# Kernel optimization log

Measured on AMD Instinct MI355X. Metric: run time of the kernel, lower is better.

## Reference

```python
import jax, jax.numpy as jnp
import numpy as np

N, E, F, H = 50000, 400000, 128, 512


def setup_inputs() -> dict:
    key = jax.random.key(0)
    k1, k2, k3 = jax.random.split(key, 3)
    x = jax.random.normal(k1, (N, F), dtype=jnp.float32)
    edge_index = jax.random.randint(k2, (2, E), 0, N, dtype=jnp.int64)
    W = jax.random.normal(k3, (H, F), dtype=jnp.float32) * 0.05  # GCNConv linear weight [out, in]
    b = jnp.zeros((H,), dtype=jnp.float32)
    alpha = jnp.full((H,), 0.25, dtype=jnp.float32)  # PReLU default init per channel
    return {"x": x, "edge_index": edge_index, "W": W, "b": b, "alpha": alpha}


def reference(x, edge_index, W, b, alpha):
    n = x.shape[0]
    # GCNConv: linear transform first (no bias inside the matmul)
    h = x @ W.T  # [N, H]
    # add self-loops (GCNConv default add_self_loops=True)
    loops = jnp.arange(n, dtype=edge_index.dtype)
    row = jnp.concatenate([edge_index[0], loops])  # source
    col = jnp.concatenate([edge_index[1], loops])  # target
    # symmetric degree normalization: deg from edge weights (all ones) summed at targets
    deg = jax.ops.segment_sum(jnp.ones_like(col, dtype=h.dtype), col, num_segments=n)
    dinv = jnp.where(deg > 0, jax.lax.rsqrt(jnp.maximum(deg, 1.0)) * (deg > 0), 0.0)
    dinv = jnp.where(deg > 0, 1.0 / jnp.sqrt(jnp.maximum(deg, 1e-12)), 0.0)
    norm = dinv[row] * dinv[col]  # [E+N]
    # gather source features, scale, scatter-add to targets
    msgs = h[row] * norm[:, None]  # [E+N, H] -- the memory-bound gather
    out = jax.ops.segment_sum(msgs, col, num_segments=n) + b  # [N, H]
    # PReLU with per-channel alpha
    return jnp.where(out > 0, out, alpha * out)
```

## Files before the change

### kernel.cpp

```cpp
#include <hip/hip_runtime.h>


#define F_IN 128
#define H_OUT 512

typedef __bf16 bf16x8 __attribute__((ext_vector_type(8)));
typedef float  f32x4  __attribute__((ext_vector_type(4)));

__global__ __launch_bounds__(256) void cast_bf16_kernel(const float* __restrict__ src,
                                                        __bf16* __restrict__ dst, int n8) {
    int i = blockIdx.x * 256 + threadIdx.x;
    if (i >= n8) return;
    float4 a = ((const float4*)src)[i * 2];
    float4 b = ((const float4*)src)[i * 2 + 1];
    bf16x8 v;
    v[0] = (__bf16)a.x; v[1] = (__bf16)a.y; v[2] = (__bf16)a.z; v[3] = (__bf16)a.w;
    v[4] = (__bf16)b.x; v[5] = (__bf16)b.y; v[6] = (__bf16)b.z; v[7] = (__bf16)b.w;
    ((bf16x8*)dst)[i] = v;
}

__global__ __launch_bounds__(256) void scale_cast_kernel(const float* __restrict__ x,
                                                         const float* __restrict__ dinv,
                                                         __bf16* __restrict__ xs, int n8) {
    int i = blockIdx.x * 256 + threadIdx.x;
    if (i >= n8) return;
    float dv = dinv[i >> 4];
    float4 a = ((const float4*)x)[i * 2];
    float4 b = ((const float4*)x)[i * 2 + 1];
    bf16x8 v;
    v[0] = (__bf16)(a.x * dv); v[1] = (__bf16)(a.y * dv);
    v[2] = (__bf16)(a.z * dv); v[3] = (__bf16)(a.w * dv);
    v[4] = (__bf16)(b.x * dv); v[5] = (__bf16)(b.y * dv);
    v[6] = (__bf16)(b.z * dv); v[7] = (__bf16)(b.w * dv);
    ((bf16x8*)xs)[i] = v;
}

__global__ __launch_bounds__(256) void count_deg_kernel(const int* __restrict__ col,
                                                        unsigned* __restrict__ deg, int E) {
    int e = blockIdx.x * 256 + threadIdx.x;
    if (e < E) atomicAdd(&deg[col[e]], 1u);
}

__global__ __launch_bounds__(256) void deg_reduce_kernel(const unsigned* __restrict__ deg,
                                                         unsigned* __restrict__ partial, int n) {
    __shared__ unsigned wsum[4];
    const int t = threadIdx.x;
    const int i0 = blockIdx.x * 1024 + t * 4;
    unsigned s = 0;
    if (i0 + 3 < n) {
        uint4 v = *(const uint4*)(deg + i0);
        s = v.x + v.y + v.z + v.w;
    } else {
        #pragma unroll
        for (int j = 0; j < 4; ++j) if (i0 + j < n) s += deg[i0 + j];
    }
    #pragma unroll
    for (int o = 32; o > 0; o >>= 1) s += __shfl_down(s, (unsigned)o, 64);
    if ((t & 63) == 0) wsum[t >> 6] = s;
    __syncthreads();
    if (t == 0) partial[blockIdx.x] = wsum[0] + wsum[1] + wsum[2] + wsum[3];
}

__global__ __launch_bounds__(64) void scan_partials_kernel(const unsigned* __restrict__ partial,
                                                           unsigned* __restrict__ offs, int nb) {
    const int t = threadIdx.x;
    unsigned v = (t < nb) ? partial[t] : 0u;
    unsigned x = v;
    #pragma unroll
    for (int o = 1; o < 64; o <<= 1) {
        unsigned y = __shfl_up(x, (unsigned)o, 64);
        if (t >= o) x += y;
    }
    if (t < nb) offs[t] = x - v;
}

__global__ __launch_bounds__(256) void scan_apply_kernel(const unsigned* __restrict__ deg,
                                                         const unsigned* __restrict__ offs,
                                                         int* __restrict__ rowptr,
                                                         float* __restrict__ dinv,
                                                         unsigned* __restrict__ cursor,
                                                         int n, int E) {
    __shared__ unsigned wsum[4];
    const int t = threadIdx.x, lane = t & 63, wid = t >> 6;
    const int i0 = blockIdx.x * 1024 + t * 4;
    unsigned d[4] = {0u, 0u, 0u, 0u};
    if (i0 + 3 < n) {
        uint4 v = *(const uint4*)(deg + i0);
        d[0] = v.x; d[1] = v.y; d[2] = v.z; d[3] = v.w;
    } else {
        #pragma unroll
        for (int j = 0; j < 4; ++j) if (i0 + j < n) d[j] = deg[i0 + j];
    }
    unsigned s = d[0] + d[1] + d[2] + d[3];
    unsigned x = s;
    #pragma unroll
    for (int o = 1; o < 64; o <<= 1) {
        unsigned y = __shfl_up(x, (unsigned)o, 64);
        if (lane >= o) x += y;
    }
    if (lane == 63) wsum[wid] = x;
    __syncthreads();
    unsigned wprev = 0;
    for (int q = 0; q < wid; ++q) wprev += wsum[q];
    unsigned base = offs[blockIdx.x] + wprev + (x - s);
    unsigned run = 0;
    #pragma unroll
    for (int j = 0; j < 4; ++j) {
        int i = i0 + j;
        if (i < n) {
            rowptr[i] = (int)(base + run);
            dinv[i]   = rsqrtf((float)(d[j] + 1u));
            cursor[i] = 0u;
        }
        run += d[j];
    }
    if (blockIdx.x == 0 && t == 0) rowptr[n] = E;
}

__global__ __launch_bounds__(256) void fill_csr_kernel(const int* __restrict__ row,
                                                       const int* __restrict__ col,
                                                       const int* __restrict__ rowptr,
                                                       unsigned* __restrict__ cursor,
                                                       int* __restrict__ adj, int E) {
    int e = blockIdx.x * 256 + threadIdx.x;
    if (e >= E) return;
    int c = col[e];
    unsigned p = atomicAdd(&cursor[c], 1u);
    adj[rowptr[c] + (int)p] = row[e];
}

__global__ __launch_bounds__(256) void gather_agg_kernel(const int* __restrict__ rowptr,
                                                         const int* __restrict__ adj,
                                                         const __bf16* __restrict__ xs,
                                                         const float* __restrict__ dinv,
                                                         __bf16* __restrict__ ag, int N) {
    const int t = threadIdx.x;
    const int node = blockIdx.x * 16 + (t >> 4);
    if (node >= N) return;
    const int li = t & 15;

    const bf16x8* xs8 = (const bf16x8*)xs;
    bf16x8 sv = xs8[(size_t)node * 16 + li];
    float acc[8];
    #pragma unroll
    for (int q = 0; q < 8; ++q) acc[q] = (float)sv[q];

    const int s = rowptr[node];
    const int e = rowptr[node + 1];
    int j = s;
    for (; j + 3 < e; j += 4) {
        int r0 = adj[j], r1 = adj[j + 1], r2 = adj[j + 2], r3 = adj[j + 3];
        bf16x8 v0 = xs8[(size_t)r0 * 16 + li];
        bf16x8 v1 = xs8[(size_t)r1 * 16 + li];
        bf16x8 v2 = xs8[(size_t)r2 * 16 + li];
        bf16x8 v3 = xs8[(size_t)r3 * 16 + li];
        #pragma unroll
        for (int q = 0; q < 8; ++q)
            acc[q] += ((float)v0[q] + (float)v1[q]) + ((float)v2[q] + (float)v3[q]);
    }
    for (; j < e; ++j) {
        int r0 = adj[j];
        bf16x8 v0 = xs8[(size_t)r0 * 16 + li];
        #pragma unroll
        for (int q = 0; q < 8; ++q) acc[q] += (float)v0[q];
    }

    const float dv = dinv[node];
    bf16x8 o;
    #pragma unroll
    for (int q = 0; q < 8; ++q) o[q] = (__bf16)(acc[q] * dv);
    ((bf16x8*)ag)[(size_t)node * 16 + li] = o;
}

__global__ __launch_bounds__(256) void gemm_mfma_kernel(const __bf16* __restrict__ ag,
                                                        const __bf16* __restrict__ Wb,
                                                        const float* __restrict__ bias,
                                                        const float* __restrict__ alpha,
                                                        float* __restrict__ out, int N) {
    __shared__ __bf16 As[128][136];
    __shared__ __bf16 Bs[128][136];

    const int rb = blockIdx.x * 128;
    const int cb = blockIdx.y * 128;
    const int t  = threadIdx.x;

    #pragma unroll
    for (int i = 0; i < 8; ++i) {
        int c  = i * 256 + t;
        int r  = c >> 4;
        int k8 = (c & 15) * 8;
        bf16x8 v;
        #pragma unroll
        for (int j = 0; j < 8; ++j) v[j] = (__bf16)0.0f;
        if (rb + r < N) v = *(const bf16x8*)(ag + (size_t)(rb + r) * F_IN + k8);
        *(bf16x8*)&As[r][k8] = v;
    }
    #pragma unroll
    for (int i = 0; i < 8; ++i) {
        int c  = i * 256 + t;
        int r  = c >> 4;
        int k8 = (c & 15) * 8;
        bf16x8 v = *(const bf16x8*)(Wb + (size_t)(cb + r) * F_IN + k8);
        *(bf16x8*)&Bs[r][k8] = v;
    }
    __syncthreads();

    const int w    = t >> 6;
    const int lane = t & 63;
    const int lrow = lane & 15;
    const int lk   = (lane >> 4) * 8;

    f32x4 acc[2][8] = {};
    #pragma unroll
    for (int ks = 0; ks < 4; ++ks) {
        const int k0 = ks * 32 + lk;
        bf16x8 a0 = *(const bf16x8*)&As[w * 32 + lrow][k0];
        bf16x8 a1 = *(const bf16x8*)&As[w * 32 + 16 + lrow][k0];
        #pragma unroll
        for (int tn = 0; tn < 8; ++tn) {
            bf16x8 bfr = *(const bf16x8*)&Bs[tn * 16 + lrow][k0];
            acc[0][tn] = __builtin_amdgcn_mfma_f32_16x16x32_bf16(a0, bfr, acc[0][tn], 0, 0, 0);
            acc[1][tn] = __builtin_amdgcn_mfma_f32_16x16x32_bf16(a1, bfr, acc[1][tn], 0, 0, 0);
        }
    }

    float bb[8], aa[8];
    #pragma unroll
    for (int tn = 0; tn < 8; ++tn) {
        int n = cb + tn * 16 + lrow;
        bb[tn] = bias[n];
        aa[tn] = alpha[n];
    }
    const int rloc = (lane >> 4) * 4;
    #pragma unroll
    for (int tm = 0; tm < 2; ++tm) {
        #pragma unroll
        for (int r = 0; r < 4; ++r) {
            int m = rb + w * 32 + tm * 16 + rloc + r;
            if (m >= N) continue;
            #pragma unroll
            for (int tn = 0; tn < 8; ++tn) {
                int n = cb + tn * 16 + lrow;
                float v = acc[tm][tn][r] + bb[tn];
                v = v > 0.f ? v : aa[tn] * v;
                out[(size_t)m * H_OUT + n] = v;
            }
        }
    }
}

extern "C" void kernel_launch(void* const* d_in, const int* in_sizes, int n_in,
                              void* d_out, int out_size, void* d_ws, size_t ws_size,
                              hipStream_t stream) {
    const float* x     = (const float*)d_in[0];
    const int*   ei    = (const int*)d_in[1];
    const float* W     = (const float*)d_in[2];
    const float* b     = (const float*)d_in[3];
    const float* alpha = (const float*)d_in[4];
    float*       out   = (float*)d_out;

    const int N = in_sizes[0] / F_IN;
    const int E = in_sizes[1] / 2;
    const int* row = ei;
    const int* col = ei + E;
    const int NB = (N + 1023) / 1024;

    char* wsb = (char*)d_ws;
    size_t off = 0;
    __bf16* xs = (__bf16*)(wsb + off);  off += (size_t)N * F_IN * 2;     off = (off + 63) & ~(size_t)63;
    __bf16* ag = (__bf16*)(wsb + off);  off += (size_t)N * F_IN * 2;     off = (off + 63) & ~(size_t)63;
    __bf16* Wb = (__bf16*)(wsb + off);  off += (size_t)H_OUT * F_IN * 2; off = (off + 63) & ~(size_t)63;
    unsigned* deg    = (unsigned*)(wsb + off);  off += (size_t)N * 4;
    unsigned* cursor = (unsigned*)(wsb + off);  off += (size_t)N * 4;
    float*    dinv   = (float*)(wsb + off);     off += (size_t)N * 4;
    int*      rowptr = (int*)(wsb + off);       off += (size_t)(N + 1) * 4;
    off = (off + 63) & ~(size_t)63;
    unsigned* partial = (unsigned*)(wsb + off); off += (size_t)NB * 4;
    unsigned* offs    = (unsigned*)(wsb + off); off += (size_t)NB * 4;
    off = (off + 63) & ~(size_t)63;
    int* adj = (int*)(wsb + off);

    hipMemsetAsync(deg, 0, (size_t)N * 4, stream);

    int nw8 = H_OUT * F_IN / 8;
    cast_bf16_kernel<<<(nw8 + 255) / 256, 256, 0, stream>>>(W, Wb, nw8);

    count_deg_kernel<<<(E + 255) / 256, 256, 0, stream>>>(col, deg, E);
    deg_reduce_kernel<<<NB, 256, 0, stream>>>(deg, partial, N);
    scan_partials_kernel<<<1, 64, 0, stream>>>(partial, offs, NB);
    scan_apply_kernel<<<NB, 256, 0, stream>>>(deg, offs, rowptr, dinv, cursor, N, E);
    fill_csr_kernel<<<(E + 255) / 256, 256, 0, stream>>>(row, col, rowptr, cursor, adj, E);

    int nx8 = N * F_IN / 8;
    scale_cast_kernel<<<(nx8 + 255) / 256, 256, 0, stream>>>(x, dinv, xs, nx8);

    gather_agg_kernel<<<(N + 15) / 16, 256, 0, stream>>>(rowptr, adj, xs, dinv, ag, N);

    dim3 ggrid((N + 127) / 128, H_OUT / 128);
    gemm_mfma_kernel<<<ggrid, 256, 0, stream>>>(ag, Wb, b, alpha, out, N);
}
```

Baseline: 220.1 us.

## Merge prep kernels, replace scan with atomic segment allocation, move dinv into gather

Fuses the W cast, the x cast and the degree counting into one launch. The three-kernel prefix scan is replaced by a per-wavefront scan that reserves its segment base with an atomic on a global counter, so CSR segments are no longer in node order. fill_csr writes straight to the cursor, and the final cursor value marks each segment's end. Because dinv is now computed after x is cast, the source-side scaling moves into the gather as a per-neighbor dinv load, which adds extra scattered loads in exchange for fewer launches.

```diff
diff --git a/kernel.cpp b/kernel.cpp
--- a/kernel.cpp
+++ b/kernel.cpp
@@ -7,129 +7,76 @@
 typedef __bf16 bf16x8 __attribute__((ext_vector_type(8)));
 typedef float  f32x4  __attribute__((ext_vector_type(4)));
 
-__global__ __launch_bounds__(256) void cast_bf16_kernel(const float* __restrict__ src,
-                                                        __bf16* __restrict__ dst, int n8) {
-    int i = blockIdx.x * 256 + threadIdx.x;
-    if (i >= n8) return;
-    float4 a = ((const float4*)src)[i * 2];
-    float4 b = ((const float4*)src)[i * 2 + 1];
-    bf16x8 v;
-    v[0] = (__bf16)a.x; v[1] = (__bf16)a.y; v[2] = (__bf16)a.z; v[3] = (__bf16)a.w;
-    v[4] = (__bf16)b.x; v[5] = (__bf16)b.y; v[6] = (__bf16)b.z; v[7] = (__bf16)b.w;
-    ((bf16x8*)dst)[i] = v;
-}
-
-__global__ __launch_bounds__(256) void scale_cast_kernel(const float* __restrict__ x,
-                                                         const float* __restrict__ dinv,
-                                                         __bf16* __restrict__ xs, int n8) {
-    int i = blockIdx.x * 256 + threadIdx.x;
-    if (i >= n8) return;
-    float dv = dinv[i >> 4];
-    float4 a = ((const float4*)x)[i * 2];
-    float4 b = ((const float4*)x)[i * 2 + 1];
-    bf16x8 v;
-    v[0] = (__bf16)(a.x * dv); v[1] = (__bf16)(a.y * dv);
-    v[2] = (__bf16)(a.z * dv); v[3] = (__bf16)(a.w * dv);
-    v[4] = (__bf16)(b.x * dv); v[5] = (__bf16)(b.y * dv);
-    v[6] = (__bf16)(b.z * dv); v[7] = (__bf16)(b.w * dv);
-    ((bf16x8*)xs)[i] = v;
-}
-
-__global__ __launch_bounds__(256) void count_deg_kernel(const int* __restrict__ col,
-                                                        unsigned* __restrict__ deg, int E) {
-    int e = blockIdx.x * 256 + threadIdx.x;
-    if (e < E) atomicAdd(&deg[col[e]], 1u);
-}
-
-__global__ __launch_bounds__(256) void deg_reduce_kernel(const unsigned* __restrict__ deg,
-                                                         unsigned* __restrict__ partial, int n) {
-    __shared__ unsigned wsum[4];
-    const int t = threadIdx.x;
-    const int i0 = blockIdx.x * 1024 + t * 4;
-    unsigned s = 0;
-    if (i0 + 3 < n) {
-        uint4 v = *(const uint4*)(deg + i0);
-        s = v.x + v.y + v.z + v.w;
+__global__ __launch_bounds__(256) void prep_kernel(const float* __restrict__ W,
+                                                   __bf16* __restrict__ Wb, int nw8,
+                                                   const float* __restrict__ x,
+                                                   __bf16* __restrict__ xs, int nx8,
+                                                   const int* __restrict__ col,
+                                                   unsigned* __restrict__ deg, int E,
+                                                   int NWB, int NXB) {
+    const int b = blockIdx.x, t = threadIdx.x;
+    if (b < NWB) {
+        int i = b * 256 + t;
+        if (i >= nw8) return;
+        float4 a0 = ((const float4*)W)[i * 2];
+        float4 a1 = ((const float4*)W)[i * 2 + 1];
+        bf16x8 v;
+        v[0] = (__bf16)a0.x; v[1] = (__bf16)a0.y; v[2] = (__bf16)a0.z; v[3] = (__bf16)a0.w;
+        v[4] = (__bf16)a1.x; v[5] = (__bf16)a1.y; v[6] = (__bf16)a1.z; v[7] = (__bf16)a1.w;
+        ((bf16x8*)Wb)[i] = v;
+    } else if (b < NWB + NXB) {
+        int i = (b - NWB) * 256 + t;
+        if (i >= nx8) return;
+        float4 a0 = ((const float4*)x)[i * 2];
+        float4 a1 = ((const float4*)x)[i * 2 + 1];
+        bf16x8 v;
+        v[0] = (__bf16)a0.x; v[1] = (__bf16)a0.y; v[2] = (__bf16)a0.z; v[3] = (__bf16)a0.w;
+        v[4] = (__bf16)a1.x; v[5] = (__bf16)a1.y; v[6] = (__bf16)a1.z; v[7] = (__bf16)a1.w;
+        ((bf16x8*)xs)[i] = v;
     } else {
-        #pragma unroll
-        for (int j = 0; j < 4; ++j) if (i0 + j < n) s += deg[i0 + j];
-    }
-    #pragma unroll
-    for (int o = 32; o > 0; o >>= 1) s += __shfl_down(s, (unsigned)o, 64);
-    if ((t & 63) == 0) wsum[t >> 6] = s;
-    __syncthreads();
-    if (t == 0) partial[blockIdx.x] = wsum[0] + wsum[1] + wsum[2] + wsum[3];
-}
-
-__global__ __launch_bounds__(64) void scan_partials_kernel(const unsigned* __restrict__ partial,
-                                                           unsigned* __restrict__ offs, int nb) {
-    const int t = threadIdx.x;
-    unsigned v = (t < nb) ? partial[t] : 0u;
-    unsigned x = v;
-    #pragma unroll
-    for (int o = 1; o < 64; o <<= 1) {
-        unsigned y = __shfl_up(x, (unsigned)o, 64);
-        if (t >= o) x += y;
-    }
-    if (t < nb) offs[t] = x - v;
-}
-
-__global__ __launch_bounds__(256) void scan_apply_kernel(const unsigned* __restrict__ deg,
-                                                         const unsigned* __restrict__ offs,
-                                                         int* __restrict__ rowptr,
-                                                         float* __restrict__ dinv,
-                                                         unsigned* __restrict__ cursor,
-                                                         int n, int E) {
-    __shared__ unsigned wsum[4];
-    const int t = threadIdx.x, lane = t & 63, wid = t >> 6;
-    const int i0 = blockIdx.x * 1024 + t * 4;
-    unsigned d[4] = {0u, 0u, 0u, 0u};
-    if (i0 + 3 < n) {
-        uint4 v = *(const uint4*)(deg + i0);
-        d[0] = v.x; d[1] = v.y; d[2] = v.z; d[3] = v.w;
-    } else {
-        #pragma unroll
-        for (int j = 0; j < 4; ++j) if (i0 + j < n) d[j] = deg[i0 + j];
-    }
-    unsigned s = d[0] + d[1] + d[2] + d[3];
-    unsigned x = s;
+        int e = (b - NWB - NXB) * 256 + t;
+        if (e < E) atomicAdd(&deg[col[e]], 1u);
+    }
+}
+
+__global__ __launch_bounds__(256) void assign_kernel(const unsigned* __restrict__ deg,
+                                                     unsigned* __restrict__ total,
+                                                     int* __restrict__ rowptr,
+                                                     unsigned* __restrict__ cursor,
+                                                     float* __restrict__ dinv, int n) {
+    const int i = blockIdx.x * 256 + threadIdx.x;
+    const int lane = threadIdx.x & 63;
+    unsigned d = (i < n) ? deg[i] : 0u;
+    unsigned x = d;
     #pragma unroll
     for (int o = 1; o < 64; o <<= 1) {
         unsigned y = __shfl_up(x, (unsigned)o, 64);
         if (lane >= o) x += y;
     }
-    if (lane == 63) wsum[wid] = x;
-    __syncthreads();
-    unsigned wprev = 0;
-    for (int q = 0; q < wid; ++q) wprev += wsum[q];
-    unsigned base = offs[blockIdx.x] + wprev + (x - s);
-    unsigned run = 0;
-    #pragma unroll
-    for (int j = 0; j < 4; ++j) {
-        int i = i0 + j;
-        if (i < n) {
-            rowptr[i] = (int)(base + run);
-            dinv[i]   = rsqrtf((float)(d[j] + 1u));
-            cursor[i] = 0u;
-        }
-        run += d[j];
-    }
-    if (blockIdx.x == 0 && t == 0) rowptr[n] = E;
+    unsigned tot = __shfl(x, 63, 64);
+    unsigned wb = 0;
+    if (lane == 63) wb = atomicAdd(total, tot);
+    wb = __shfl(wb, 63, 64);
+    if (i < n) {
+        unsigned start = wb + x - d;
+        rowptr[i] = (int)start;
+        cursor[i] = start;
+        dinv[i]   = rsqrtf((float)(d + 1u));
+    }
 }
 
 __global__ __launch_bounds__(256) void fill_csr_kernel(const int* __restrict__ row,
                                                        const int* __restrict__ col,
-                                                       const int* __restrict__ rowptr,
                                                        unsigned* __restrict__ cursor,
                                                        int* __restrict__ adj, int E) {
     int e = blockIdx.x * 256 + threadIdx.x;
     if (e >= E) return;
-    int c = col[e];
-    unsigned p = atomicAdd(&cursor[c], 1u);
-    adj[rowptr[c] + (int)p] = row[e];
+    unsigned p = atomicAdd(&cursor[col[e]], 1u);
+    adj[p] = row[e];
 }
 
 __global__ __launch_bounds__(256) void gather_agg_kernel(const int* __restrict__ rowptr,
+                                                         const unsigned* __restrict__ cursor,
                                                          const int* __restrict__ adj,
                                                          const __bf16* __restrict__ xs,
                                                          const float* __restrict__ dinv,
@@ -140,35 +87,38 @@
     const int li = t & 15;
 
     const bf16x8* xs8 = (const bf16x8*)xs;
+    const float dvn = dinv[node];
     bf16x8 sv = xs8[(size_t)node * 16 + li];
     float acc[8];
     #pragma unroll
-    for (int q = 0; q < 8; ++q) acc[q] = (float)sv[q];
+    for (int q = 0; q < 8; ++q) acc[q] = dvn * (float)sv[q];
 
     const int s = rowptr[node];
-    const int e = rowptr[node + 1];
+    const int e = (int)cursor[node];
     int j = s;
     for (; j + 3 < e; j += 4) {
         int r0 = adj[j], r1 = adj[j + 1], r2 = adj[j + 2], r3 = adj[j + 3];
+        float w0 = dinv[r0], w1 = dinv[r1], w2 = dinv[r2], w3 = dinv[r3];
         bf16x8 v0 = xs8[(size_t)r0 * 16 + li];
         bf16x8 v1 = xs8[(size_t)r1 * 16 + li];
         bf16x8 v2 = xs8[(size_t)r2 * 16 + li];
         bf16x8 v3 = xs8[(size_t)r3 * 16 + li];
         #pragma unroll
         for (int q = 0; q < 8; ++q)
-            acc[q] += ((float)v0[q] + (float)v1[q]) + ((float)v2[q] + (float)v3[q]);
+            acc[q] += (w0 * (float)v0[q] + w1 * (float)v1[q]) +
+                      (w2 * (float)v2[q] + w3 * (float)v3[q]);
     }
     for (; j < e; ++j) {
         int r0 = adj[j];
+        float w0 = dinv[r0];
         bf16x8 v0 = xs8[(size_t)r0 * 16 + li];
         #pragma unroll
-        for (int q = 0; q < 8; ++q) acc[q] += (float)v0[q];
-    }
-
-    const float dv = dinv[node];
+        for (int q = 0; q < 8; ++q) acc[q] += w0 * (float)v0[q];
+    }
+
     bf16x8 o;
     #pragma unroll
-    for (int q = 0; q < 8; ++q) o[q] = (__bf16)(acc[q] * dv);
+    for (int q = 0; q < 8; ++q) o[q] = (__bf16)(acc[q] * dvn);
     ((bf16x8*)ag)[(size_t)node * 16 + li] = o;
 }
 
@@ -263,39 +213,32 @@
     const int E = in_sizes[1] / 2;
     const int* row = ei;
     const int* col = ei + E;
-    const int NB = (N + 1023) / 1024;
 
     char* wsb = (char*)d_ws;
     size_t off = 0;
     __bf16* xs = (__bf16*)(wsb + off);  off += (size_t)N * F_IN * 2;     off = (off + 63) & ~(size_t)63;
     __bf16* ag = (__bf16*)(wsb + off);  off += (size_t)N * F_IN * 2;     off = (off + 63) & ~(size_t)63;
     __bf16* Wb = (__bf16*)(wsb + off);  off += (size_t)H_OUT * F_IN * 2; off = (off + 63) & ~(size_t)63;
-    unsigned* deg    = (unsigned*)(wsb + off);  off += (size_t)N * 4;
+    unsigned* deg    = (unsigned*)(wsb + off);  off += (size_t)(N + 1) * 4;
     unsigned* cursor = (unsigned*)(wsb + off);  off += (size_t)N * 4;
     float*    dinv   = (float*)(wsb + off);     off += (size_t)N * 4;
-    int*      rowptr = (int*)(wsb + off);       off += (size_t)(N + 1) * 4;
-    off = (off + 63) & ~(size_t)63;
-    unsigned* partial = (unsigned*)(wsb + off); off += (size_t)NB * 4;
-    unsigned* offs    = (unsigned*)(wsb + off); off += (size_t)NB * 4;
+    int*      rowptr = (int*)(wsb + off);       off += (size_t)N * 4;
     off = (off + 63) & ~(size_t)63;
     int* adj = (int*)(wsb + off);
-
-    hipMemsetAsync(deg, 0, (size_t)N * 4, stream);
-
-    int nw8 = H_OUT * F_IN / 8;
-    cast_bf16_kernel<<<(nw8 + 255) / 256, 256, 0, stream>>>(W, Wb, nw8);
-
-    count_deg_kernel<<<(E + 255) / 256, 256, 0, stream>>>(col, deg, E);
-    deg_reduce_kernel<<<NB, 256, 0, stream>>>(deg, partial, N);
-    scan_partials_kernel<<<1, 64, 0, stream>>>(partial, offs, NB);
-    scan_apply_kernel<<<NB, 256, 0, stream>>>(deg, offs, rowptr, dinv, cursor, N, E);
-    fill_csr_kernel<<<(E + 255) / 256, 256, 0, stream>>>(row, col, rowptr, cursor, adj, E);
-
-    int nx8 = N * F_IN / 8;
-    scale_cast_kernel<<<(nx8 + 255) / 256, 256, 0, stream>>>(x, dinv, xs, nx8);
-
-    gather_agg_kernel<<<(N + 15) / 16, 256, 0, stream>>>(rowptr, adj, xs, dinv, ag, N);
-
+    unsigned* total = deg + N;
+
+    const int nw8 = H_OUT * F_IN / 8;
+    const int nx8 = N * F_IN / 8;
+    const int NWB = (nw8 + 255) / 256;
+    const int NXB = (nx8 + 255) / 256;
+    const int NEB = (E + 255) / 256;
+
+    hipMemsetAsync(deg, 0, (size_t)(N + 1) * 4, stream);
+    prep_kernel<<<NWB + NXB + NEB, 256, 0, stream>>>(W, Wb, nw8, x, xs, nx8,
+                                                     col, deg, E, NWB, NXB);
+    assign_kernel<<<(N + 255) / 256, 256, 0, stream>>>(deg, total, rowptr, cursor, dinv, N);
+    fill_csr_kernel<<<(E + 255) / 256, 256, 0, stream>>>(row, col, cursor, adj, E);
+    gather_agg_kernel<<<(N + 15) / 16, 256, 0, stream>>>(rowptr, cursor, adj, xs, dinv, ag, N);
     dim3 ggrid((N + 127) / 128, H_OUT / 128);
     gemm_mfma_kernel<<<ggrid, 256, 0, stream>>>(ag, Wb, b, alpha, out, N);
 }
```

After: 219.5 us. About the same (-0.3%).
